# Performance work log

Hardware: AMD Instinct MI355X
Metric: run time of the kernel (lower is better)

The kernel has to match this reference:

```python
import jax, jax.numpy as jnp
import numpy as np

N, E = 50000, 800000
IN_F, HID, OUT_F, K = 128, 128, 64, 3
LAMBDA_MAX = 2.0  # standard upper bound for normalized-Laplacian eigenvalues (dgl.laplacian_lambda_max)
BN_EPS = 1e-5


def setup_inputs() -> dict:
    key = jax.random.key(0)
    ks = jax.random.split(key, 8)
    s = 0.05
    features = jax.random.normal(ks[0], (N, IN_F), jnp.float32)
    src = jax.random.randint(ks[1], (E,), 0, N)
    dst = jax.random.randint(ks[2], (E,), 0, N)
    W1 = jax.random.normal(ks[3], (HID, K * IN_F), jnp.float32) * s
    b1 = jnp.zeros((HID,), jnp.float32)
    W3 = jax.random.normal(ks[4], (HID, K * HID), jnp.float32) * s
    b3 = jnp.zeros((HID,), jnp.float32)
    gamma = jnp.ones((HID,), jnp.float32)
    beta = jnp.zeros((HID,), jnp.float32)
    Wm1 = jax.random.normal(ks[5], (HID, HID), jnp.float32) * s
    bm1 = jnp.zeros((HID,), jnp.float32)
    Wm2 = jax.random.normal(ks[6], (OUT_F, HID), jnp.float32) * s
    bm2 = jnp.zeros((OUT_F,), jnp.float32)
    return dict(features=features, src=src, dst=dst, W1=W1, b1=b1, W3=W3, b3=b3,
                gamma=gamma, beta=beta, Wm1=Wm1, bm1=bm1, Wm2=Wm2, bm2=bm2)


def chebconv(feat, src, dst, d_invsqrt, W, b, k):
    """DGL ChebConv: T_0 = X, T_1 = Lhat X, T_i = 2 Lhat T_{i-1} - T_{i-2};
    Lhat = (2/lam) (I - Ahat) - I, Ahat = D^{-1/2} A D^{-1/2}; linear over concat of orders."""
    re_norm = 2.0 / LAMBDA_MAX
    n = feat.shape[0]

    def spmv(x):  # Ahat @ x via edge gather (src) + segment-sum scatter (dst)
        return jax.ops.segment_sum((x * d_invsqrt)[src], dst, num_segments=n) * d_invsqrt

    Xs = [feat]
    if k > 1:
        h = spmv(feat)
        Xs.append(-re_norm * h + feat * (re_norm - 1.0))
    for _ in range(2, k):
        h = spmv(Xs[-1])
        Xs.append(-2.0 * re_norm * h + Xs[-1] * (2.0 * (re_norm - 1.0)) - Xs[-2])
    return jnp.concatenate(Xs, axis=1) @ W.T + b  # [N, k*d] @ [d_out, k*d]^T


def reference(features, src, dst, W1, b1, W3, b3, gamma, beta, Wm1, bm1, Wm2, bm2):
    n = features.shape[0]
    in_deg = jax.ops.segment_sum(jnp.ones((src.shape[0],), jnp.float32), dst, num_segments=n)
    d_invsqrt = (jnp.clip(in_deg, 1.0, None) ** -0.5)[:, None]

    x = jax.nn.relu(chebconv(features, src, dst, d_invsqrt, W1, b1, K))
    # BatchNorm1d (training-mode batch stats, biased variance)
    mu = x.mean(axis=0)
    var = x.var(axis=0)
    x = (x - mu) * jax.lax.rsqrt(var + BN_EPS) * gamma + beta
    # NOTE: the source's Chebyshev early-stopping loop computes cheb2(x) repeatedly but
    # never reassigns `x`, so it is output-inert and omitted (same math).
    x_res = x
    x = jax.nn.relu(chebconv(x, src, dst, d_invsqrt, W3, b3, K))
    x = x + x_res  # dropout in eval mode == identity
    h = jax.nn.relu(x @ Wm1.T + bm1)
    return h @ Wm2.T + bm2
```

## Files before the change

kernel.cpp:

```cpp
#include <hip/hip_runtime.h>
#include <hip/hip_bf16.h>
#include <math.h>

#define NF 128

typedef unsigned short ushort8 __attribute__((ext_vector_type(8)));
typedef float f32x4 __attribute__((ext_vector_type(4)));
typedef _Float16 half8 __attribute__((ext_vector_type(8)));

static inline int ceil_div(int a, int b) { return (a + b - 1) / b; }

__global__ __launch_bounds__(256) void bucket_hist_kernel(const int* __restrict__ dst,
                                                          int* __restrict__ counts,
                                                          int e, int nblk, int nbuck) {
  __shared__ int h[256];
  int t = threadIdx.x, blk = blockIdx.x;
  h[t] = 0;
  __syncthreads();
  int base = blk * 4096;
#pragma unroll
  for (int k = 0; k < 16; ++k) {
    int i = base + k * 256 + t;
    if (i < e) atomicAdd(&h[dst[i] >> 8], 1);
  }
  __syncthreads();
  for (int b = t; b < nbuck; b += 256) counts[b * nblk + blk] = h[b];
}

__global__ __launch_bounds__(256) void bucket_scan_rows_kernel(int* __restrict__ counts,
                                                               int* __restrict__ btot,
                                                               int nblk) {
  __shared__ int sh[256];
  int b = blockIdx.x, t = threadIdx.x;
  int* row = counts + (size_t)b * nblk;
  int carry = 0;
  for (int base = 0; base < nblk; base += 256) {
    int v = (base + t < nblk) ? row[base + t] : 0;
    sh[t] = v;
    __syncthreads();
    for (int off = 1; off < 256; off <<= 1) {
      int add = (t >= off) ? sh[t - off] : 0;
      __syncthreads();
      sh[t] += add;
      __syncthreads();
    }
    if (base + t < nblk) row[base + t] = carry + sh[t] - v;
    carry += sh[255];
    __syncthreads();
  }
  if (t == 0) btot[b] = carry;
}

__global__ __launch_bounds__(256) void bucket_base_kernel(const int* __restrict__ btot,
                                                          int* __restrict__ bbase,
                                                          int nbuck, int e) {
  __shared__ int sh[256];
  __shared__ int carry;
  int t = threadIdx.x;
  if (t == 0) carry = 0;
  __syncthreads();
  for (int base = 0; base < nbuck; base += 256) {
    int v = (base + t < nbuck) ? btot[base + t] : 0;
    sh[t] = v;
    __syncthreads();
    for (int off = 1; off < 256; off <<= 1) {
      int add = (t >= off) ? sh[t - off] : 0;
      __syncthreads();
      sh[t] += add;
      __syncthreads();
    }
    if (base + t < nbuck) bbase[base + t] = carry + sh[t] - v;
    __syncthreads();
    if (t == 0) carry += sh[255];
    __syncthreads();
  }
  if (t == 0) bbase[nbuck] = e;
}

__global__ __launch_bounds__(256) void bucket_bin_kernel(const int* __restrict__ src,
                                                         const int* __restrict__ dst,
                                                         const int* __restrict__ counts,
                                                         const int* __restrict__ bbase,
                                                         int2* __restrict__ binned,
                                                         int e, int nblk, int nbuck) {
  __shared__ int cur[256];
  int t = threadIdx.x, blk = blockIdx.x;
  for (int b = t; b < nbuck; b += 256) cur[b] = counts[b * nblk + blk] + bbase[b];
  __syncthreads();
  int base = blk * 4096;
#pragma unroll
  for (int k = 0; k < 16; ++k) {
    int i = base + k * 256 + t;
    if (i < e) {
      int d = dst[i];
      int pos = atomicAdd(&cur[d >> 8], 1);
      binned[pos] = make_int2(src[i], d);
    }
  }
}

__global__ __launch_bounds__(256) void bucket_finalize_kernel(const int2* __restrict__ binned,
                                                              const int* __restrict__ bbase,
                                                              int* __restrict__ offsets,
                                                              int* __restrict__ csr,
                                                              float* __restrict__ dinv,
                                                              float* __restrict__ dsq,
                                                              int n, int e, int nbuck) {
  __shared__ int deg[256];
  __shared__ int offs[256];
  __shared__ int cur[256];
  int b = blockIdx.x, t = threadIdx.x;
  int ebeg = bbase[b];
  int eend = bbase[b + 1];
  deg[t] = 0;
  __syncthreads();
  for (int j = ebeg + t; j < eend; j += 256) atomicAdd(&deg[binned[j].y & 255], 1);
  __syncthreads();
  int v = deg[t];
  offs[t] = v;
  __syncthreads();
  for (int off = 1; off < 256; off <<= 1) {
    int add = (t >= off) ? offs[t - off] : 0;
    __syncthreads();
    offs[t] += add;
    __syncthreads();
  }
  int excl = offs[t] - v;
  cur[t] = excl;
  int node = b * 256 + t;
  if (node < n) {
    offsets[node] = ebeg + excl;
    float d = (float)(v > 1 ? v : 1);
    dinv[node] = rsqrtf(d);
    dsq[node] = sqrtf(d);
  }
  if (b == nbuck - 1 && t == 0) offsets[n] = e;
  __syncthreads();
  for (int j = ebeg + t; j < eend; j += 256) {
    int2 pr = binned[j];
    int pos = atomicAdd(&cur[pr.y & 255], 1);
    csr[ebeg + pos] = pr.x;
  }
}


__global__ void prep_feat_kernel(const float* __restrict__ feat, const float* __restrict__ dinv,
                                 _Float16* __restrict__ Fsp, _Float16* __restrict__ xs,
                                 int n) {
  int i = blockIdx.x * 256 + threadIdx.x;
  if (i >= n * 16) return;
  int row = i >> 4, fc = i & 15;
  const float4* s = (const float4*)(feat + (size_t)row * NF + fc * 8);
  float4 a = s[0], b = s[1];
  float xv[8] = {a.x, a.y, a.z, a.w, b.x, b.y, b.z, b.w};
  float d = dinv[row];
  half8 h, f;
#pragma unroll
  for (int j = 0; j < 8; ++j) { h[j] = (_Float16)(xv[j] * d); f[j] = (_Float16)xv[j]; }
  *(half8*)(xs + (size_t)row * NF + fc * 8) = h;
  int swz = (fc ^ (row & 15)) * 8;
  *(half8*)(Fsp + (size_t)row * 128 + swz) = f;
}

__global__ __launch_bounds__(256) void spmv_kernel(
    const _Float16* __restrict__ xs16, const float* __restrict__ dinv,
    const int* __restrict__ offsets, const int* __restrict__ csr,
    const _Float16* __restrict__ zs16, const float* __restrict__ dsq, float a, float bz,
    _Float16* __restrict__ outsp, _Float16* __restrict__ outs16, int n) {
  int w = threadIdx.x >> 6, lane = threadIdx.x & 63;
  int node = blockIdx.x * 4 + w;
  if (node >= n) return;
  int beg = __builtin_amdgcn_readfirstlane(offsets[node]);
  int end = __builtin_amdgcn_readfirstlane(offsets[node + 1]);
  int eh = lane >> 4;
  int cq = lane & 15;

  float acc[8];
#pragma unroll
  for (int j = 0; j < 8; ++j) acc[j] = 0.f;

  int e2 = beg;
  for (; e2 + 8 <= end; e2 += 8) {
    int s0 = csr[e2 + eh];
    int s1 = csr[e2 + 4 + eh];
    half8 g0 = ((const half8*)(xs16 + (size_t)s0 * NF))[cq];
    half8 g1 = ((const half8*)(xs16 + (size_t)s1 * NF))[cq];
#pragma unroll
    for (int j = 0; j < 8; ++j) acc[j] += (float)g0[j];
#pragma unroll
    for (int j = 0; j < 8; ++j) acc[j] += (float)g1[j];
  }
  for (; e2 + 4 <= end; e2 += 4) {
    int s0 = csr[e2 + eh];
    half8 g0 = ((const half8*)(xs16 + (size_t)s0 * NF))[cq];
#pragma unroll
    for (int j = 0; j < 8; ++j) acc[j] += (float)g0[j];
  }
  int rem = end - e2;
  if (eh < rem) {
    int s0 = csr[e2 + eh];
    half8 g0 = ((const half8*)(xs16 + (size_t)s0 * NF))[cq];
#pragma unroll
    for (int j = 0; j < 8; ++j) acc[j] += (float)g0[j];
  }
#pragma unroll
  for (int j = 0; j < 8; ++j) {
    acc[j] += __shfl_xor(acc[j], 16);
    acc[j] += __shfl_xor(acc[j], 32);
  }
  if (eh == 0) {
    float dv = dinv[node];
    float v[8];
#pragma unroll
    for (int j = 0; j < 8; ++j) v[j] = a * dv * acc[j];
    if (zs16) {
      float zf = bz * dsq[node];
      half8 zz = ((const half8*)(zs16 + (size_t)node * NF))[cq];
#pragma unroll
      for (int j = 0; j < 8; ++j) v[j] += zf * (float)zz[j];
    }
    half8 ho, hs;
#pragma unroll
    for (int j = 0; j < 8; ++j) { ho[j] = (_Float16)v[j]; hs[j] = (_Float16)(v[j] * dv); }
    int swz = (cq ^ (node & 15)) * 8;
    *(half8*)(outsp + (size_t)node * 128 + swz) = ho;
    if (outs16) *(half8*)(outs16 + (size_t)node * NF + cq * 8) = hs;
  }
}

__device__ __forceinline__ void pack_one(const float* __restrict__ W, ushort8* __restrict__ Wp,
                                         int f, int NT, int K) {
  int lane = f & 63;
  int hl = (f >> 6) & 1;
  int rest = f >> 7;
  int nt = rest % NT;
  int kunit = rest / NT;
  int nrow = nt * 16 + (lane & 15);
  int k0 = kunit * 32 + (lane >> 4) * 8;
  const float* srcp = W + (size_t)nrow * K + k0;
  ushort8 v;
#pragma unroll
  for (int j = 0; j < 8; ++j) {
    float x = srcp[j];
    _Float16 h = (_Float16)x;
    if (hl) h = (_Float16)(x - (float)h);
    v[j] = __builtin_bit_cast(unsigned short, h);
  }
  Wp[f] = v;
}

__global__ void pack_all_kernel(const float* __restrict__ W1, ushort8* __restrict__ P1,
                                const float* __restrict__ W3, ushort8* __restrict__ P3,
                                const float* __restrict__ Wm1, ushort8* __restrict__ PM1,
                                const float* __restrict__ Wm2, ushort8* __restrict__ PM2) {
  int f = blockIdx.x * 256 + threadIdx.x;
  if (f < 12288) pack_one(W1, P1, f, 8, 384);
  else if (f < 24576) pack_one(W3, P3, f - 12288, 8, 384);
  else if (f < 28672) pack_one(Wm1, PM1, f - 24576, 8, 128);
  else if (f < 30720) pack_one(Wm2, PM2, f - 28672, 4, 128);
}


__device__ __forceinline__ void stage_sp(const _Float16* gsrc, float4* lbuf, int tid) {
  const char* g = (const char*)gsrc;
  char* l = (char*)lbuf;
#pragma unroll
  for (int k = 0; k < 2; ++k) {
    int off = k * 8192 + tid * 16;
    __builtin_amdgcn_global_load_lds(
        (const __attribute__((address_space(1))) void*)(g + off),
        (__attribute__((address_space(3))) void*)(l + off), 16, 0, 0);
  }
}

__device__ __forceinline__ void lds_put16(_Float16* L, int row, int col, float v) {
  L[row * 128 + (((col >> 3) ^ (row & 15)) << 3) + (col & 7)] = (_Float16)v;
}

struct Bchunk {
  ushort8 h[2][2];
  ushort8 l[2][2];
};

__device__ __forceinline__ void loadB(const ushort8* __restrict__ Wp, int kunit0,
                                      int lane, int wn, Bchunk& c) {
#pragma unroll
  for (int k2 = 0; k2 < 2; ++k2) {
#pragma unroll
    for (int j = 0; j < 2; ++j) {
      const ushort8* bp = Wp + (size_t)((kunit0 + k2) * 8 + wn * 2 + j) * 128 + lane;
      c.h[k2][j] = bp[0];
      c.l[k2][j] = bp[64];
    }
  }
}

__device__ __forceinline__ void mfma_chunk(const float4* A4, const Bchunk& c, int kbase,
                                           int lane, int wm, f32x4 (*acc)[2]) {
#pragma unroll
  for (int k2 = 0; k2 < 2; ++k2) {
    int kunit = kbase + k2;
    half8 a[2];
#pragma unroll
    for (int mt = 0; mt < 2; ++mt) {
      int arow = wm * 32 + mt * 16 + (lane & 15);
      int fc = (kunit & 3) * 4 + (lane >> 4);
      a[mt] = __builtin_bit_cast(half8, A4[arow * 16 + (fc ^ (arow & 15))]);
    }
#pragma unroll
    for (int j = 0; j < 2; ++j) {
      half8 bh = __builtin_bit_cast(half8, c.h[k2][j]);
      half8 bl = __builtin_bit_cast(half8, c.l[k2][j]);
#pragma unroll
      for (int mt = 0; mt < 2; ++mt) {
        acc[mt][j] = __builtin_amdgcn_mfma_f32_16x16x32_f16(a[mt], bh, acc[mt][j], 0, 0, 0);
        acc[mt][j] = __builtin_amdgcn_mfma_f32_16x16x32_f16(a[mt], bl, acc[mt][j], 0, 0, 0);
      }
    }
  }
}

template<int NT, int NT2>
__device__ __forceinline__ void gemm_step16(const float4* A4, const ushort8* __restrict__ Wp,
                                            int kunit, int lane, int wm, int wn,
                                            f32x4 (*acc)[NT2]) {
  half8 a[2];
#pragma unroll
  for (int mt = 0; mt < 2; ++mt) {
    int arow = wm * 32 + mt * 16 + (lane & 15);
    int fc = (kunit & 3) * 4 + (lane >> 4);
    a[mt] = __builtin_bit_cast(half8, A4[arow * 16 + (fc ^ (arow & 15))]);
  }
#pragma unroll
  for (int j = 0; j < NT2; ++j) {
    int nt = wn * NT2 + j;
    const ushort8* bp = Wp + (size_t)(kunit * NT + nt) * 2 * 64 + lane;
    half8 bh = __builtin_bit_cast(half8, bp[0]);
    half8 bl = __builtin_bit_cast(half8, bp[64]);
#pragma unroll
    for (int mt = 0; mt < 2; ++mt) {
      acc[mt][j] = __builtin_amdgcn_mfma_f32_16x16x32_f16(a[mt], bh, acc[mt][j], 0, 0, 0);
      acc[mt][j] = __builtin_amdgcn_mfma_f32_16x16x32_f16(a[mt], bl, acc[mt][j], 0, 0, 0);
    }
  }
}

__device__ __forceinline__ void gemm3_pipeline(const _Float16* A0, const _Float16* A1,
                                               const _Float16* A2, const ushort8* Wp,
                                               float4 (*buf)[1024], size_t r0,
                                               int tid, int lane, int wm, int wn,
                                               f32x4 (*acc)[2]) {
  const _Float16* Aarr[3] = {A0, A1, A2};
  stage_sp(A0 + r0 * 128, buf[0], tid);
  Bchunk bc0, bc1;
#pragma unroll
  for (int p = 0; p < 3; ++p) {
    loadB(Wp, p * 4, lane, wn, bc0);
    loadB(Wp, p * 4 + 2, lane, wn, bc1);
    if (p + 1 < 3) stage_sp(Aarr[p + 1] + r0 * 128, buf[(p + 1) & 1], tid);
    asm volatile("s_waitcnt vmcnt(10)" ::: "memory");
    __builtin_amdgcn_s_barrier();
    __builtin_amdgcn_sched_barrier(0);
    mfma_chunk(buf[p & 1], bc0, p * 4, lane, wm, acc);
    mfma_chunk(buf[p & 1], bc1, p * 4 + 2, lane, wm, acc);
    __builtin_amdgcn_sched_barrier(0);
    __builtin_amdgcn_s_barrier();
  }
}

__global__ __launch_bounds__(512, 4) void conv1_gemm_kernel(
    const _Float16* __restrict__ A0, const _Float16* __restrict__ A1,
    const _Float16* __restrict__ A2,
    const ushort8* __restrict__ Wp, const float* __restrict__ bias,
    _Float16* __restrict__ Xh, float* __restrict__ stats, int n) {
  __shared__ float4 buf[2][1024];
  __shared__ float sstat[256];

  int tid = threadIdx.x;
  int lane = tid & 63, wid = tid >> 6;
  int wm = wid >> 2, wn = wid & 3;
  size_t r0 = (size_t)blockIdx.x * 64;

  f32x4 acc[2][2];
#pragma unroll
  for (int mt = 0; mt < 2; ++mt)
#pragma unroll
    for (int j = 0; j < 2; ++j) acc[mt][j] = (f32x4)0.f;

  gemm3_pipeline(A0, A1, A2, Wp, buf, r0, tid, lane, wm, wn, acc);

  if (tid < 256) sstat[tid] = 0.f;
  __syncthreads();
#pragma unroll
  for (int mt = 0; mt < 2; ++mt) {
    int rbase = (int)r0 + wm * 32 + mt * 16 + (lane >> 4) * 4;
#pragma unroll
    for (int j = 0; j < 2; ++j) {
      int col = wn * 32 + j * 16 + (lane & 15);
      float b = bias[col];
      float sj = 0.f, qj = 0.f;
#pragma unroll
      for (int i = 0; i < 4; ++i) {
        int row = rbase + i;
        if (row < n) {
          float v = fmaxf(acc[mt][j][i] + b, 0.f);
          Xh[(size_t)row * NF + col] = (_Float16)v;
          sj += v; qj += v * v;
        }
      }
      sj += __shfl_xor(sj, 16); sj += __shfl_xor(sj, 32);
      qj += __shfl_xor(qj, 16); qj += __shfl_xor(qj, 32);
      if ((lane >> 4) == 0) {
        atomicAdd(&sstat[col], sj);
        atomicAdd(&sstat[128 + col], qj);
      }
    }
  }
  __syncthreads();
  if (tid < 256) atomicAdd(&stats[(blockIdx.x & 7) * 256 + tid], sstat[tid]);
}

__global__ __launch_bounds__(512, 4) void fused_tail_kernel(
    const _Float16* __restrict__ Xsp, const _Float16* __restrict__ T1sp,
    const _Float16* __restrict__ T2sp,
    const _Float16* __restrict__ xsA, const float* __restrict__ dsq,
    const ushort8* __restrict__ Wp3, const float* __restrict__ b3,
    const ushort8* __restrict__ WpM1, const float* __restrict__ bm1,
    const ushort8* __restrict__ WpM2, const float* __restrict__ bm2,
    float* __restrict__ out, int n) {
  __shared__ float4 buf[2][1024];
  _Float16* L = (_Float16*)buf[0];

  int tid = threadIdx.x;
  int lane = tid & 63, wid = tid >> 6;
  int wm = wid >> 2, wn = wid & 3;
  size_t r0 = (size_t)blockIdx.x * 64;

  f32x4 acc[2][2];
#pragma unroll
  for (int mt = 0; mt < 2; ++mt)
#pragma unroll
    for (int j = 0; j < 2; ++j) acc[mt][j] = (f32x4)0.f;

  gemm3_pipeline(Xsp, T1sp, T2sp, Wp3, buf, r0, tid, lane, wm, wn, acc);

#pragma unroll
  for (int mt = 0; mt < 2; ++mt) {
    int rb = wm * 32 + mt * 16 + (lane >> 4) * 4;
#pragma unroll
    for (int j = 0; j < 2; ++j) {
      int col = wn * 32 + j * 16 + (lane & 15);
      float b = b3[col];
#pragma unroll
      for (int i = 0; i < 4; ++i) {
        int lrow = rb + i;
        int row = (int)r0 + lrow;
        float v = 0.f;
        if (row < n) {
          float xres = (float)xsA[(size_t)row * NF + col] * dsq[row];
          v = fmaxf(acc[mt][j][i] + b, 0.f) + xres;
        }
        lds_put16(L, lrow, col, v);
      }
    }
  }
  __syncthreads();
  f32x4 acc2[2][2];
#pragma unroll
  for (int mt = 0; mt < 2; ++mt)
#pragma unroll
    for (int j = 0; j < 2; ++j) acc2[mt][j] = (f32x4)0.f;
#pragma unroll
  for (int ks = 0; ks < 4; ++ks)
    gemm_step16<8, 2>(buf[0], WpM1, ks, lane, wm, wn, acc2);
  __syncthreads();
#pragma unroll
  for (int mt = 0; mt < 2; ++mt) {
    int rb = wm * 32 + mt * 16 + (lane >> 4) * 4;
#pragma unroll
    for (int j = 0; j < 2; ++j) {
      int col = wn * 32 + j * 16 + (lane & 15);
      float b = bm1[col];
#pragma unroll
      for (int i = 0; i < 4; ++i) {
        float v = fmaxf(acc2[mt][j][i] + b, 0.f);
        lds_put16(L, rb + i, col, v);
      }
    }
  }
  __syncthreads();
  f32x4 acc3[2][1];
#pragma unroll
  for (int mt = 0; mt < 2; ++mt) acc3[mt][0] = (f32x4)0.f;
#pragma unroll
  for (int ks = 0; ks < 4; ++ks)
    gemm_step16<4, 1>(buf[0], WpM2, ks, lane, wm, wn, acc3);
#pragma unroll
  for (int mt = 0; mt < 2; ++mt) {
    int rb = wm * 32 + mt * 16 + (lane >> 4) * 4;
    int col = wn * 16 + (lane & 15);
    float b = bm2[col];
#pragma unroll
    for (int i = 0; i < 4; ++i) {
      int row = (int)r0 + rb + i;
      if (row < n) out[(size_t)row * 64 + col] = acc3[mt][0][i] + b;
    }
  }
}

__global__ void bn_apply_kernel(const _Float16* __restrict__ Xh, const float* __restrict__ stats,
                                const float* __restrict__ gamma, const float* __restrict__ beta,
                                const float* __restrict__ dinv,
                                _Float16* __restrict__ Xsp, _Float16* __restrict__ xs16,
                                float fn, int n) {
  int i = blockIdx.x * 256 + threadIdx.x;
  if (i >= n * 16) return;
  int row = i >> 4, fc = i & 15;
  half8 xh = *(const half8*)(Xh + (size_t)row * NF + fc * 8);
  float xv[8];
  int c0 = fc * 8;
#pragma unroll
  for (int j = 0; j < 8; ++j) {
    int c = c0 + j;
    float s1 = 0.f, s2 = 0.f;
#pragma unroll
    for (int r = 0; r < 8; ++r) {
      s1 += stats[r * 256 + c];
      s2 += stats[r * 256 + NF + c];
    }
    float mu = s1 / fn;
    float var = s2 / fn - mu * mu;
    float s = gamma[c] * rsqrtf(var + 1e-5f);
    xv[j] = ((float)xh[j] - mu) * s + beta[c];
  }
  float d = dinv[row];
  half8 hs, hu;
#pragma unroll
  for (int j = 0; j < 8; ++j) { hs[j] = (_Float16)(xv[j] * d); hu[j] = (_Float16)xv[j]; }
  *(half8*)(xs16 + (size_t)row * NF + fc * 8) = hs;
  int swz = (fc ^ (row & 15)) * 8;
  *(half8*)(Xsp + (size_t)row * 128 + swz) = hu;
}

extern "C" void kernel_launch(void* const* d_in, const int* in_sizes, int n_in,
                              void* d_out, int out_size, void* d_ws, size_t ws_size,
                              hipStream_t stream) {
  const float* feat  = (const float*)d_in[0];
  const int*   src   = (const int*)d_in[1];
  const int*   dst   = (const int*)d_in[2];
  const float* W1    = (const float*)d_in[3];
  const float* b1    = (const float*)d_in[4];
  const float* W3    = (const float*)d_in[5];
  const float* b3    = (const float*)d_in[6];
  const float* gamma = (const float*)d_in[7];
  const float* beta  = (const float*)d_in[8];
  const float* Wm1   = (const float*)d_in[9];
  const float* bm1   = (const float*)d_in[10];
  const float* Wm2   = (const float*)d_in[11];
  const float* bm2   = (const float*)d_in[12];
  int n = in_sizes[0] / NF;
  int e = in_sizes[1];

  char* p = (char*)d_ws;
  auto alloc = [&](size_t bytes) {
    char* r = p;
    p += (bytes + 255) & ~size_t(255);
    return r;
  };
  int nblk  = ceil_div(e, 4096);
  int nbuck = ceil_div(n, 256);

  float* dinv     = (float*)alloc((size_t)n * 4);
  float* dsq      = (float*)alloc((size_t)n * 4);
  int*   offsets  = (int*)alloc((size_t)(n + 1) * 4);
  int*   counts   = (int*)alloc((size_t)nblk * nbuck * 4);
  int*   btot     = (int*)alloc((size_t)nbuck * 4);
  int*   bbase    = (int*)alloc((size_t)(nbuck + 1) * 4);
  int*   csr      = (int*)alloc((size_t)e * 4);
  float* stats    = (float*)alloc(8 * 256 * 4);
  ushort8* Wp1  = (ushort8*)alloc(12 * 8 * 2 * 64 * 16);
  ushort8* Wp3  = (ushort8*)alloc(12 * 8 * 2 * 64 * 16);
  ushort8* WpM1 = (ushort8*)alloc(4 * 8 * 2 * 64 * 16);
  ushort8* WpM2 = (ushort8*)alloc(4 * 4 * 2 * 64 * 16);
  size_t spb = (size_t)(n + 64) * 256;
  _Float16* Fsp  = (_Float16*)alloc(spb);
  _Float16* T1sp = (_Float16*)alloc(spb);
  _Float16* T2sp = (_Float16*)alloc(spb);
  _Float16* Xsp  = (_Float16*)alloc(spb);
  _Float16* Xh   = (_Float16*)alloc((size_t)n * NF * 2);
  _Float16* xsA  = (_Float16*)alloc((size_t)n * NF * 2);
  _Float16* xsB  = (_Float16*)alloc((size_t)n * NF * 2);
  int2* binned = (int2*)Fsp;

  hipMemsetAsync(stats, 0, 8 * 256 * 4, stream);

  int fb = ceil_div(n * 16, 256);
  int sb = ceil_div(n, 4);
  int gb = ceil_div(n, 64);

  bucket_hist_kernel<<<nblk, 256, 0, stream>>>(dst, counts, e, nblk, nbuck);
  bucket_scan_rows_kernel<<<nbuck, 256, 0, stream>>>(counts, btot, nblk);
  bucket_base_kernel<<<1, 256, 0, stream>>>(btot, bbase, nbuck, e);
  bucket_bin_kernel<<<nblk, 256, 0, stream>>>(src, dst, counts, bbase, binned, e, nblk, nbuck);
  bucket_finalize_kernel<<<nbuck, 256, 0, stream>>>(binned, bbase, offsets, csr, dinv, dsq, n, e, nbuck);

  pack_all_kernel<<<120, 256, 0, stream>>>(W1, Wp1, W3, Wp3, Wm1, WpM1, Wm2, WpM2);

  prep_feat_kernel<<<fb, 256, 0, stream>>>(feat, dinv, Fsp, xsA, n);
  spmv_kernel<<<sb, 256, 0, stream>>>(xsA, dinv, offsets, csr, nullptr, nullptr, -1.f, 0.f, T1sp, xsB, n);
  spmv_kernel<<<sb, 256, 0, stream>>>(xsB, dinv, offsets, csr, xsA, dsq, -2.f, -1.f, T2sp, nullptr, n);
  conv1_gemm_kernel<<<gb, 512, 0, stream>>>(Fsp, T1sp, T2sp, Wp1, b1, Xh, stats, n);

  bn_apply_kernel<<<fb, 256, 0, stream>>>(Xh, stats, gamma, beta, dinv, Xsp, xsA, (float)n, n);

  spmv_kernel<<<sb, 256, 0, stream>>>(xsA, dinv, offsets, csr, nullptr, nullptr, -1.f, 0.f, T1sp, xsB, n);
  spmv_kernel<<<sb, 256, 0, stream>>>(xsB, dinv, offsets, csr, xsA, dsq, -2.f, -1.f, T2sp, nullptr, n);

  fused_tail_kernel<<<gb, 512, 0, stream>>>(Xsp, T1sp, T2sp, xsA, dsq, Wp3, b3, WpM1, bm1,
                                            WpM2, bm2, (float*)d_out, n);
}
```

Measured before the change: 267.5 us.

## Drop prescaled fp16 copies; SpMV gathers swizzled buffers and applies dinv per edge

The SpMV now gathers directly from the swizzled GEMM-operand buffers (Fsp/T1sp/Xsp) and multiplies each neighbor by its dinv, instead of reading a separate dinv-prescaled fp16 copy. This removes the xsA/xsB arrays, the dsq array, and the extra writes in prep, bn_apply and SpMV. The tail GEMM's K order is rotated (weights packed with rot=4) so the Xsp chunk is loaded last and its LDS tile can be reused as the residual. The cost is an extra per-edge dinv gather and a multiply inside the SpMV inner loop.

```diff
diff --git a/kernel.cpp b/kernel.cpp
--- a/kernel.cpp
+++ b/kernel.cpp
@@ -104,7 +104,6 @@
                                                               int* __restrict__ offsets,
                                                               int* __restrict__ csr,
                                                               float* __restrict__ dinv,
-                                                              float* __restrict__ dsq,
                                                               int n, int e, int nbuck) {
   __shared__ int deg[256];
   __shared__ int offs[256];
@@ -132,7 +131,6 @@
     offsets[node] = ebeg + excl;
     float d = (float)(v > 1 ? v : 1);
     dinv[node] = rsqrtf(d);
-    dsq[node] = sqrtf(d);
   }
   if (b == nbuck - 1 && t == 0) offsets[n] = e;
   __syncthreads();
@@ -144,29 +142,26 @@
 }
 
 
-__global__ void prep_feat_kernel(const float* __restrict__ feat, const float* __restrict__ dinv,
-                                 _Float16* __restrict__ Fsp, _Float16* __restrict__ xs,
-                                 int n) {
+__global__ void prep_feat_kernel(const float* __restrict__ feat,
+                                 _Float16* __restrict__ Fsp, int n) {
   int i = blockIdx.x * 256 + threadIdx.x;
   if (i >= n * 16) return;
   int row = i >> 4, fc = i & 15;
   const float4* s = (const float4*)(feat + (size_t)row * NF + fc * 8);
   float4 a = s[0], b = s[1];
   float xv[8] = {a.x, a.y, a.z, a.w, b.x, b.y, b.z, b.w};
-  float d = dinv[row];
-  half8 h, f;
-#pragma unroll
-  for (int j = 0; j < 8; ++j) { h[j] = (_Float16)(xv[j] * d); f[j] = (_Float16)xv[j]; }
-  *(half8*)(xs + (size_t)row * NF + fc * 8) = h;
+  half8 f;
+#pragma unroll
+  for (int j = 0; j < 8; ++j) f[j] = (_Float16)xv[j];
   int swz = (fc ^ (row & 15)) * 8;
   *(half8*)(Fsp + (size_t)row * 128 + swz) = f;
 }
 
 __global__ __launch_bounds__(256) void spmv_kernel(
-    const _Float16* __restrict__ xs16, const float* __restrict__ dinv,
+    const _Float16* __restrict__ xsp, const float* __restrict__ dinv,
     const int* __restrict__ offsets, const int* __restrict__ csr,
-    const _Float16* __restrict__ zs16, const float* __restrict__ dsq, float a, float bz,
-    _Float16* __restrict__ outsp, _Float16* __restrict__ outs16, int n) {
+    const _Float16* __restrict__ zsp, float a, float bz,
+    _Float16* __restrict__ outsp, int n) {
   int w = threadIdx.x >> 6, lane = threadIdx.x & 63;
   int node = blockIdx.x * 4 + w;
   if (node >= n) return;
@@ -183,25 +178,28 @@
   for (; e2 + 8 <= end; e2 += 8) {
     int s0 = csr[e2 + eh];
     int s1 = csr[e2 + 4 + eh];
-    half8 g0 = ((const half8*)(xs16 + (size_t)s0 * NF))[cq];
-    half8 g1 = ((const half8*)(xs16 + (size_t)s1 * NF))[cq];
-#pragma unroll
-    for (int j = 0; j < 8; ++j) acc[j] += (float)g0[j];
-#pragma unroll
-    for (int j = 0; j < 8; ++j) acc[j] += (float)g1[j];
+    float w0 = dinv[s0], w1 = dinv[s1];
+    half8 g0 = *(const half8*)(xsp + (size_t)s0 * 128 + ((cq ^ (s0 & 15)) << 3));
+    half8 g1 = *(const half8*)(xsp + (size_t)s1 * 128 + ((cq ^ (s1 & 15)) << 3));
+#pragma unroll
+    for (int j = 0; j < 8; ++j) acc[j] += w0 * (float)g0[j];
+#pragma unroll
+    for (int j = 0; j < 8; ++j) acc[j] += w1 * (float)g1[j];
   }
   for (; e2 + 4 <= end; e2 += 4) {
     int s0 = csr[e2 + eh];
-    half8 g0 = ((const half8*)(xs16 + (size_t)s0 * NF))[cq];
-#pragma unroll
-    for (int j = 0; j < 8; ++j) acc[j] += (float)g0[j];
+    float w0 = dinv[s0];
+    half8 g0 = *(const half8*)(xsp + (size_t)s0 * 128 + ((cq ^ (s0 & 15)) << 3));
+#pragma unroll
+    for (int j = 0; j < 8; ++j) acc[j] += w0 * (float)g0[j];
   }
   int rem = end - e2;
   if (eh < rem) {
     int s0 = csr[e2 + eh];
-    half8 g0 = ((const half8*)(xs16 + (size_t)s0 * NF))[cq];
-#pragma unroll
-    for (int j = 0; j < 8; ++j) acc[j] += (float)g0[j];
+    float w0 = dinv[s0];
+    half8 g0 = *(const half8*)(xsp + (size_t)s0 * 128 + ((cq ^ (s0 & 15)) << 3));
+#pragma unroll
+    for (int j = 0; j < 8; ++j) acc[j] += w0 * (float)g0[j];
   }
 #pragma unroll
   for (int j = 0; j < 8; ++j) {
@@ -209,34 +207,34 @@
     acc[j] += __shfl_xor(acc[j], 32);
   }
   if (eh == 0) {
-    float dv = dinv[node];
+    float dv = a * dinv[node];
     float v[8];
 #pragma unroll
-    for (int j = 0; j < 8; ++j) v[j] = a * dv * acc[j];
-    if (zs16) {
-      float zf = bz * dsq[node];
-      half8 zz = ((const half8*)(zs16 + (size_t)node * NF))[cq];
-#pragma unroll
-      for (int j = 0; j < 8; ++j) v[j] += zf * (float)zz[j];
-    }
-    half8 ho, hs;
-#pragma unroll
-    for (int j = 0; j < 8; ++j) { ho[j] = (_Float16)v[j]; hs[j] = (_Float16)(v[j] * dv); }
-    int swz = (cq ^ (node & 15)) * 8;
+    for (int j = 0; j < 8; ++j) v[j] = dv * acc[j];
+    int swz = (cq ^ (node & 15)) << 3;
+    if (zsp) {
+      half8 zz = *(const half8*)(zsp + (size_t)node * 128 + swz);
+#pragma unroll
+      for (int j = 0; j < 8; ++j) v[j] += bz * (float)zz[j];
+    }
+    half8 ho;
+#pragma unroll
+    for (int j = 0; j < 8; ++j) ho[j] = (_Float16)v[j];
     *(half8*)(outsp + (size_t)node * 128 + swz) = ho;
-    if (outs16) *(half8*)(outs16 + (size_t)node * NF + cq * 8) = hs;
   }
 }
 
 __device__ __forceinline__ void pack_one(const float* __restrict__ W, ushort8* __restrict__ Wp,
-                                         int f, int NT, int K) {
+                                         int f, int NT, int K, int rot) {
   int lane = f & 63;
   int hl = (f >> 6) & 1;
   int rest = f >> 7;
   int nt = rest % NT;
   int kunit = rest / NT;
+  int nK = K >> 5;
+  int srcKunit = (kunit + rot) % nK;
   int nrow = nt * 16 + (lane & 15);
-  int k0 = kunit * 32 + (lane >> 4) * 8;
+  int k0 = srcKunit * 32 + (lane >> 4) * 8;
   const float* srcp = W + (size_t)nrow * K + k0;
   ushort8 v;
 #pragma unroll
@@ -254,10 +252,10 @@
                                 const float* __restrict__ Wm1, ushort8* __restrict__ PM1,
                                 const float* __restrict__ Wm2, ushort8* __restrict__ PM2) {
   int f = blockIdx.x * 256 + threadIdx.x;
-  if (f < 12288) pack_one(W1, P1, f, 8, 384);
-  else if (f < 24576) pack_one(W3, P3, f - 12288, 8, 384);
-  else if (f < 28672) pack_one(Wm1, PM1, f - 24576, 8, 128);
-  else if (f < 30720) pack_one(Wm2, PM2, f - 28672, 4, 128);
+  if (f < 12288) pack_one(W1, P1, f, 8, 384, 0);
+  else if (f < 24576) pack_one(W3, P3, f - 12288, 8, 384, 4);
+  else if (f < 28672) pack_one(Wm1, PM1, f - 24576, 8, 128, 0);
+  else if (f < 30720) pack_one(Wm2, PM2, f - 28672, 4, 128, 0);
 }
 
 
@@ -273,8 +271,8 @@
   }
 }
 
-__device__ __forceinline__ void lds_put16(_Float16* L, int row, int col, float v) {
-  L[row * 128 + (((col >> 3) ^ (row & 15)) << 3) + (col & 7)] = (_Float16)v;
+__device__ __forceinline__ int lds_off16(int row, int col) {
+  return row * 128 + (((col >> 3) ^ (row & 15)) << 3) + (col & 7);
 }
 
 struct Bchunk {
@@ -421,9 +419,8 @@
 }
 
 __global__ __launch_bounds__(512, 4) void fused_tail_kernel(
-    const _Float16* __restrict__ Xsp, const _Float16* __restrict__ T1sp,
-    const _Float16* __restrict__ T2sp,
-    const _Float16* __restrict__ xsA, const float* __restrict__ dsq,
+    const _Float16* __restrict__ T1sp, const _Float16* __restrict__ T2sp,
+    const _Float16* __restrict__ Xsp,
     const ushort8* __restrict__ Wp3, const float* __restrict__ b3,
     const ushort8* __restrict__ WpM1, const float* __restrict__ bm1,
     const ushort8* __restrict__ WpM2, const float* __restrict__ bm2,
@@ -442,7 +439,7 @@
 #pragma unroll
     for (int j = 0; j < 2; ++j) acc[mt][j] = (f32x4)0.f;
 
-  gemm3_pipeline(Xsp, T1sp, T2sp, Wp3, buf, r0, tid, lane, wm, wn, acc);
+  gemm3_pipeline(T1sp, T2sp, Xsp, Wp3, buf, r0, tid, lane, wm, wn, acc);
 
 #pragma unroll
   for (int mt = 0; mt < 2; ++mt) {
@@ -454,13 +451,10 @@
 #pragma unroll
       for (int i = 0; i < 4; ++i) {
         int lrow = rb + i;
-        int row = (int)r0 + lrow;
-        float v = 0.f;
-        if (row < n) {
-          float xres = (float)xsA[(size_t)row * NF + col] * dsq[row];
-          v = fmaxf(acc[mt][j][i] + b, 0.f) + xres;
-        }
-        lds_put16(L, lrow, col, v);
+        int off = lds_off16(lrow, col);
+        float xres = (float)L[off];
+        float v = fmaxf(acc[mt][j][i] + b, 0.f) + xres;
+        L[off] = (_Float16)v;
       }
     }
   }
@@ -484,7 +478,7 @@
 #pragma unroll
       for (int i = 0; i < 4; ++i) {
         float v = fmaxf(acc2[mt][j][i] + b, 0.f);
-        lds_put16(L, rb + i, col, v);
+        L[lds_off16(rb + i, col)] = (_Float16)v;
       }
     }
   }
@@ -510,14 +504,12 @@
 
 __global__ void bn_apply_kernel(const _Float16* __restrict__ Xh, const float* __restrict__ stats,
                                 const float* __restrict__ gamma, const float* __restrict__ beta,
-                                const float* __restrict__ dinv,
-                                _Float16* __restrict__ Xsp, _Float16* __restrict__ xs16,
-                                float fn, int n) {
+                                _Float16* __restrict__ Xsp, float fn, int n) {
   int i = blockIdx.x * 256 + threadIdx.x;
   if (i >= n * 16) return;
   int row = i >> 4, fc = i & 15;
   half8 xh = *(const half8*)(Xh + (size_t)row * NF + fc * 8);
-  float xv[8];
+  half8 hu;
   int c0 = fc * 8;
 #pragma unroll
   for (int j = 0; j < 8; ++j) {
@@ -531,13 +523,8 @@
     float mu = s1 / fn;
     float var = s2 / fn - mu * mu;
     float s = gamma[c] * rsqrtf(var + 1e-5f);
-    xv[j] = ((float)xh[j] - mu) * s + beta[c];
-  }
-  float d = dinv[row];
-  half8 hs, hu;
-#pragma unroll
-  for (int j = 0; j < 8; ++j) { hs[j] = (_Float16)(xv[j] * d); hu[j] = (_Float16)xv[j]; }
-  *(half8*)(xs16 + (size_t)row * NF + fc * 8) = hs;
+    hu[j] = (_Float16)(((float)xh[j] - mu) * s + beta[c]);
+  }
   int swz = (fc ^ (row & 15)) * 8;
   *(half8*)(Xsp + (size_t)row * 128 + swz) = hu;
 }
@@ -571,7 +558,6 @@
   int nbuck = ceil_div(n, 256);
 
   float* dinv     = (float*)alloc((size_t)n * 4);
-  float* dsq      = (float*)alloc((size_t)n * 4);
   int*   offsets  = (int*)alloc((size_t)(n + 1) * 4);
   int*   counts   = (int*)alloc((size_t)nblk * nbuck * 4);
   int*   btot     = (int*)alloc((size_t)nbuck * 4);
@@ -588,8 +574,6 @@
   _Float16* T2sp = (_Float16*)alloc(spb);
   _Float16* Xsp  = (_Float16*)alloc(spb);
   _Float16* Xh   = (_Float16*)alloc((size_t)n * NF * 2);
-  _Float16* xsA  = (_Float16*)alloc((size_t)n * NF * 2);
-  _Float16* xsB  = (_Float16*)alloc((size_t)n * NF * 2);
   int2* binned = (int2*)Fsp;
 
   hipMemsetAsync(stats, 0, 8 * 256 * 4, stream);
@@ -602,20 +586,20 @@
   bucket_scan_rows_kernel<<<nbuck, 256, 0, stream>>>(counts, btot, nblk);
   bucket_base_kernel<<<1, 256, 0, stream>>>(btot, bbase, nbuck, e);
   bucket_bin_kernel<<<nblk, 256, 0, stream>>>(src, dst, counts, bbase, binned, e, nblk, nbuck);
-  bucket_finalize_kernel<<<nbuck, 256, 0, stream>>>(binned, bbase, offsets, csr, dinv, dsq, n, e, nbuck);
+  bucket_finalize_kernel<<<nbuck, 256, 0, stream>>>(binned, bbase, offsets, csr, dinv, n, e, nbuck);
 
   pack_all_kernel<<<120, 256, 0, stream>>>(W1, Wp1, W3, Wp3, Wm1, WpM1, Wm2, WpM2);
 
-  prep_feat_kernel<<<fb, 256, 0, stream>>>(feat, dinv, Fsp, xsA, n);
-  spmv_kernel<<<sb, 256, 0, stream>>>(xsA, dinv, offsets, csr, nullptr, nullptr, -1.f, 0.f, T1sp, xsB, n);
-  spmv_kernel<<<sb, 256, 0, stream>>>(xsB, dinv, offsets, csr, xsA, dsq, -2.f, -1.f, T2sp, nullptr, n);
+  prep_feat_kernel<<<fb, 256, 0, stream>>>(feat, Fsp, n);
+  spmv_kernel<<<sb, 256, 0, stream>>>(Fsp, dinv, offsets, csr, nullptr, -1.f, 0.f, T1sp, n);
+  spmv_kernel<<<sb, 256, 0, stream>>>(T1sp, dinv, offsets, csr, Fsp, -2.f, -1.f, T2sp, n);
   conv1_gemm_kernel<<<gb, 512, 0, stream>>>(Fsp, T1sp, T2sp, Wp1, b1, Xh, stats, n);
 
-  bn_apply_kernel<<<fb, 256, 0, stream>>>(Xh, stats, gamma, beta, dinv, Xsp, xsA, (float)n, n);
-
-  spmv_kernel<<<sb, 256, 0, stream>>>(xsA, dinv, offsets, csr, nullptr, nullptr, -1.f, 0.f, T1sp, xsB, n);
-  spmv_kernel<<<sb, 256, 0, stream>>>(xsB, dinv, offsets, csr, xsA, dsq, -2.f, -1.f, T2sp, nullptr, n);
-
-  fused_tail_kernel<<<gb, 512, 0, stream>>>(Xsp, T1sp, T2sp, xsA, dsq, Wp3, b3, WpM1, bm1,
+  bn_apply_kernel<<<fb, 256, 0, stream>>>(Xh, stats, gamma, beta, Xsp, (float)n, n);
+
+  spmv_kernel<<<sb, 256, 0, stream>>>(Xsp, dinv, offsets, csr, nullptr, -1.f, 0.f, T1sp, n);
+  spmv_kernel<<<sb, 256, 0, stream>>>(T1sp, dinv, offsets, csr, Xsp, -2.f, -1.f, T2sp, n);
+
+  fused_tail_kernel<<<gb, 512, 0, stream>>>(T1sp, T2sp, Xsp, Wp3, b3, WpM1, bm1,
                                             WpM2, bm2, (float*)d_out, n);
 }
```

Result: faster. 254.8 us (-4.8%).
